# Kernel optimization log

Measured on AMD Instinct MI355X. Metric: run time of the kernel, lower is better.

Reference implementation:

```python
import jax, jax.numpy as jnp
import numpy as np

HEADS = 8
DIM_HEAD = 64
SCALE = DIM_HEAD ** -0.5


def setup_inputs() -> dict:
    key = jax.random.key(0)
    k1, k2, k3, k4 = jax.random.split(key, 4)
    b, dim, l = 4, 256, 2048
    hidden = HEADS * DIM_HEAD  # 512
    x = jax.random.normal(k1, (b, dim, l), dtype=jnp.float32)
    w_qkv = jax.random.normal(k2, (3 * hidden, dim), dtype=jnp.float32) * (dim ** -0.5)
    w_out = jax.random.normal(k3, (dim, hidden), dtype=jnp.float32) * (hidden ** -0.5)
    b_out = jax.random.normal(k4, (dim,), dtype=jnp.float32) * 0.01
    return {"x": x, "w_qkv": w_qkv, "w_out": w_out, "b_out": b_out}


def reference(x, w_qkv, w_out, b_out):
    b, c, l = x.shape
    hidden = HEADS * DIM_HEAD
    # 1x1 conv == pointwise linear over channels
    qkv = jnp.einsum('oc,bcl->bol', w_qkv, x)  # [b, 3*hidden, l]
    q, k, v = jnp.split(qkv, 3, axis=1)
    def to_heads(t):
        return t.reshape(b, HEADS, DIM_HEAD, l)  # b h d l
    q, k, v = to_heads(q), to_heads(k), to_heads(v)
    q = q * SCALE
    sim = jnp.einsum('bhdi,bhdj->bhij', q, k)      # [b, h, l, l]
    attn = jax.nn.softmax(sim, axis=-1)
    out = jnp.einsum('bhij,bhdj->bhid', attn, v)   # [b, h, l, d]
    out = out.transpose(0, 1, 3, 2).reshape(b, hidden, l)  # b (h d) l
    return jnp.einsum('oc,bcl->bol', w_out, out) + b_out[None, :, None]
```

## Files before the change

### kernel.cpp

```cpp
#include <hip/hip_runtime.h>
#include <math.h>

#define Bn   4
#define Cc   256
#define Ll   2048
#define Hh   8
#define Dd   64
#define HID  512
#define OQKV 1536

typedef _Float16 half4v __attribute__((ext_vector_type(4)));
typedef _Float16 half8v __attribute__((ext_vector_type(8)));
typedef float    f32x16 __attribute__((ext_vector_type(16)));

__global__ __launch_bounds__(256) void conv_w(const float* __restrict__ wqkv,
                                              const float* __restrict__ wout,
                                              _Float16* __restrict__ wqkvh,
                                              _Float16* __restrict__ wouth) {
  int idx = blockIdx.x * 256 + threadIdx.x;
  int stride = gridDim.x * 256;
  for (int i = idx; i < OQKV * Cc; i += stride) {
    float v = wqkv[i];
    if (i < HID * Cc) v *= 0.125f;
    wqkvh[i] = (_Float16)v;
  }
  for (int i = idx; i < Cc * HID; i += stride) wouth[i] = (_Float16)wout[i];
}

__global__ __launch_bounds__(256) void conv_xT(const float* __restrict__ x,
                                               _Float16* __restrict__ xT) {
  __shared__ _Float16 T[64][72];
  const int l0 = blockIdx.x * 64, c0 = blockIdx.y * 64, bz = blockIdx.z;
  const int t = threadIdx.x;
  const float* xb = x + ((size_t)bz * Cc + c0) * Ll + l0;
  {
    int cl = t >> 2;
    int lq = (t & 3) * 16;
#pragma unroll
    for (int i = 0; i < 16; i += 4) {
      float4 v = *(const float4*)&xb[(size_t)cl * Ll + lq + i];
      T[lq + i + 0][cl] = (_Float16)v.x;
      T[lq + i + 1][cl] = (_Float16)v.y;
      T[lq + i + 2][cl] = (_Float16)v.z;
      T[lq + i + 3][cl] = (_Float16)v.w;
    }
  }
  __syncthreads();
  {
    int ll = t >> 2;
    int cq = (t & 3) * 16;
    _Float16* dst = xT + ((size_t)bz * Ll + l0 + ll) * Cc + c0 + cq;
    *(half8v*)&dst[0] = *(const half8v*)&T[ll][cq];
    *(half8v*)&dst[8] = *(const half8v*)&T[ll][cq + 8];
  }
}

template <int MODE>
__global__ __launch_bounds__(256) void gemm_f16(
    const _Float16* __restrict__ A, const _Float16* __restrict__ B,
    const float* __restrict__ bias, void* __restrict__ C, int M, int K) {
  __shared__ _Float16 As[128][40];
  __shared__ _Float16 Bs[128][40];
  const int bz = blockIdx.z;
  const int m0 = blockIdx.y * 128, n0 = blockIdx.x * 128;
  const int t = threadIdx.x;
  const int w = t >> 6, lane = t & 63, lid = lane & 31, lh = lane >> 5;
  const int mw = (w >> 1) * 64, nw = (w & 1) * 64;
  const _Float16* Bb = B + (size_t)bz * Ll * K;

  f32x16 acc[2][2];
#pragma unroll
  for (int a = 0; a < 2; ++a)
#pragma unroll
    for (int b2 = 0; b2 < 2; ++b2)
#pragma unroll
      for (int r = 0; r < 16; ++r) acc[a][b2][r] = 0.0f;

  for (int k0 = 0; k0 < K; k0 += 32) {
    for (int c = t; c < 512; c += 256) {
      int row = c >> 2, kc = (c & 3) * 8;
      *(half8v*)&As[row][kc] = *(const half8v*)&A[(size_t)(m0 + row) * K + k0 + kc];
      *(half8v*)&Bs[row][kc] = *(const half8v*)&Bb[(size_t)(n0 + row) * K + k0 + kc];
    }
    __syncthreads();
#pragma unroll
    for (int kq = 0; kq < 2; ++kq) {
      half8v af[2], bf[2];
#pragma unroll
      for (int ms = 0; ms < 2; ++ms)
        af[ms] = *(const half8v*)&As[mw + ms * 32 + lid][kq * 16 + 8 * lh];
#pragma unroll
      for (int ns = 0; ns < 2; ++ns)
        bf[ns] = *(const half8v*)&Bs[nw + ns * 32 + lid][kq * 16 + 8 * lh];
#pragma unroll
      for (int ms = 0; ms < 2; ++ms)
#pragma unroll
        for (int ns = 0; ns < 2; ++ns)
          acc[ms][ns] = __builtin_amdgcn_mfma_f32_32x32x16_f16(af[ms], bf[ns], acc[ms][ns], 0, 0, 0);
    }
    __syncthreads();
  }
#pragma unroll
  for (int ms = 0; ms < 2; ++ms)
#pragma unroll
    for (int ns = 0; ns < 2; ++ns)
#pragma unroll
      for (int r = 0; r < 16; ++r) {
        int row = m0 + mw + ms * 32 + (r & 3) + 8 * (r >> 2) + 4 * lh;
        int col = n0 + nw + ns * 32 + lid;
        float v = acc[ms][ns][r];
        if (MODE == 1) {
          ((float*)C)[((size_t)bz * M + row) * Ll + col] = v + bias[row];
        } else {
          ((_Float16*)C)[((size_t)bz * M + row) * Ll + col] = (_Float16)v;
        }
      }
}

__global__ __launch_bounds__(256) void attn_f16(const _Float16* __restrict__ qkv,
                                                _Float16* __restrict__ aoutT) {
  const int b = blockIdx.z, h = blockIdx.y;
  const int i0 = blockIdx.x * 128;
  const int t = threadIdx.x;
  const int w = t >> 6, lane = t & 63, lid = lane & 31, lh = lane >> 5;
  const _Float16* qb = qkv + ((size_t)b * OQKV + h * Dd) * Ll;
  const _Float16* kb = qb + (size_t)HID * Ll;
  const _Float16* vb = qb + (size_t)(2 * HID) * Ll;

  __shared__ _Float16 Qs[128][72];
  __shared__ _Float16 Ks[64][72];
  __shared__ _Float16 Vs[64][72];
  __shared__ _Float16 Ps[128][72];

  {
    int il4 = (t & 15) * 4;
    int dl = (t >> 4) * 4;
#pragma unroll
    for (int half2 = 0; half2 < 2; ++half2) {
      int il = half2 * 64 + il4;
      half4v rows[4];
#pragma unroll
      for (int r = 0; r < 4; ++r)
        rows[r] = *(const half4v*)&qb[(size_t)(dl + r) * Ll + i0 + il];
#pragma unroll
      for (int c = 0; c < 4; ++c) {
        half4v o;
        o[0] = rows[0][c]; o[1] = rows[1][c]; o[2] = rows[2][c]; o[3] = rows[3][c];
        *(half4v*)&Qs[il + c][dl] = o;
      }
    }
  }
  __syncthreads();

  half8v qf[4];
#pragma unroll
  for (int kq = 0; kq < 4; ++kq)
    qf[kq] = *(const half8v*)&Qs[32 * w + lid][kq * 16 + 8 * lh];

  float lsum = 0.0f;
  f32x16 oacc[2];
#pragma unroll
  for (int ds = 0; ds < 2; ++ds)
#pragma unroll
    for (int r = 0; r < 16; ++r) oacc[ds][r] = 0.0f;

  for (int j0 = 0; j0 < Ll; j0 += 64) {
    __syncthreads();
    {
      int jl = (t & 15) * 4, dl = (t >> 4) * 4;
      half4v rows[4];
#pragma unroll
      for (int r = 0; r < 4; ++r)
        rows[r] = *(const half4v*)&kb[(size_t)(dl + r) * Ll + j0 + jl];
#pragma unroll
      for (int c = 0; c < 4; ++c) {
        half4v o;
        o[0] = rows[0][c]; o[1] = rows[1][c]; o[2] = rows[2][c]; o[3] = rows[3][c];
        *(half4v*)&Ks[jl + c][dl] = o;
      }
    }
    {
      int dl = t >> 2, jl = (t & 3) * 16;
      *(half8v*)&Vs[dl][jl]     = *(const half8v*)&vb[(size_t)dl * Ll + j0 + jl];
      *(half8v*)&Vs[dl][jl + 8] = *(const half8v*)&vb[(size_t)dl * Ll + j0 + jl + 8];
    }
    __syncthreads();

#pragma unroll
    for (int ms = 0; ms < 2; ++ms) {
      f32x16 s;
#pragma unroll
      for (int r = 0; r < 16; ++r) s[r] = 0.0f;
#pragma unroll
      for (int kq = 0; kq < 4; ++kq) {
        half8v kf = *(const half8v*)&Ks[ms * 32 + lid][kq * 16 + 8 * lh];
        s = __builtin_amdgcn_mfma_f32_32x32x16_f16(kf, qf[kq], s, 0, 0, 0);
      }
#pragma unroll
      for (int g = 0; g < 4; ++g) {
        half4v pk;
#pragma unroll
        for (int c = 0; c < 4; ++c) {
          float p = __expf(s[4 * g + c] - 3.0f);
          lsum += p;
          pk[c] = (_Float16)p;
        }
        *(half4v*)&Ps[32 * w + lid][ms * 32 + 8 * g + 4 * lh] = pk;
      }
    }
    __syncthreads();

#pragma unroll
    for (int ds = 0; ds < 2; ++ds)
#pragma unroll
      for (int jq = 0; jq < 4; ++jq) {
        half8v vf = *(const half8v*)&Vs[ds * 32 + lid][jq * 16 + 8 * lh];
        half8v pf = *(const half8v*)&Ps[32 * w + lid][jq * 16 + 8 * lh];
        oacc[ds] = __builtin_amdgcn_mfma_f32_32x32x16_f16(vf, pf, oacc[ds], 0, 0, 0);
      }
  }

  lsum += __shfl_xor(lsum, 32);
  float inv = 1.0f / lsum;
  _Float16* dst = aoutT + ((size_t)b * Ll + i0 + 32 * w + lid) * HID + h * Dd;
#pragma unroll
  for (int ds = 0; ds < 2; ++ds)
#pragma unroll
    for (int g = 0; g < 4; ++g) {
      int d = ds * 32 + 8 * g + 4 * lh;
      half4v o;
#pragma unroll
      for (int c = 0; c < 4; ++c) o[c] = (_Float16)(oacc[ds][4 * g + c] * inv);
      *(half4v*)&dst[d] = o;
    }
}

extern "C" void kernel_launch(void* const* d_in, const int* in_sizes, int n_in,
                              void* d_out, int out_size, void* d_ws, size_t ws_size,
                              hipStream_t stream) {
  const float* x     = (const float*)d_in[0];
  const float* w_qkv = (const float*)d_in[1];
  const float* w_out = (const float*)d_in[2];
  const float* b_out = (const float*)d_in[3];
  float* out = (float*)d_out;

  char* ws = (char*)d_ws;
  _Float16* xT     = (_Float16*)(ws);
  _Float16* wqkvh  = (_Float16*)(ws + 4194304);
  _Float16* wouth  = (_Float16*)(ws + 4980736);
  _Float16* qkvh   = (_Float16*)(ws + 5242880);
  _Float16* aoutT  = (_Float16*)(ws + 30408704);

  dim3 blk(256);
  conv_w<<<512, blk, 0, stream>>>(w_qkv, w_out, wqkvh, wouth);
  conv_xT<<<dim3(Ll / 64, Cc / 64, Bn), blk, 0, stream>>>(x, xT);
  gemm_f16<0><<<dim3(Ll / 128, OQKV / 128, Bn), blk, 0, stream>>>(
      wqkvh, xT, nullptr, qkvh, OQKV, Cc);
  attn_f16<<<dim3(Ll / 128, Hh, Bn), blk, 0, stream>>>(qkvh, aoutT);
  gemm_f16<1><<<dim3(Ll / 128, Cc / 128, Bn), blk, 0, stream>>>(
      wouth, aoutT, b_out, out, Cc, HID);
}
```

Measured before the change: 162.8 us.

## Double-buffer K/V in attention, keep P in registers, swizzle LDS, fuse conversions

The attention kernel now double-buffers the K and V tiles: the next tile's global loads are issued into registers before the current tile's MFMAs and written to LDS afterwards, so there is one barrier per iteration instead of three. The P shared-memory round trip is removed by packing the exp results to fp16 and exchanging halves between lanes with shuffles so they form the B operand directly. Q and K tiles get an XOR swizzle to cut LDS bank conflicts, and s_setprio hints are placed around the MFMA blocks. The weight and x conversion kernels are merged into one launch, at the cost of more registers and LDS per block, which may lower occupancy.

```diff
diff --git a/kernel.cpp b/kernel.cpp
--- a/kernel.cpp
+++ b/kernel.cpp
@@ -13,25 +13,25 @@
 typedef _Float16 half8v __attribute__((ext_vector_type(8)));
 typedef float    f32x16 __attribute__((ext_vector_type(16)));
 
-__global__ __launch_bounds__(256) void conv_w(const float* __restrict__ wqkv,
-                                              const float* __restrict__ wout,
-                                              _Float16* __restrict__ wqkvh,
-                                              _Float16* __restrict__ wouth) {
-  int idx = blockIdx.x * 256 + threadIdx.x;
-  int stride = gridDim.x * 256;
-  for (int i = idx; i < OQKV * Cc; i += stride) {
-    float v = wqkv[i];
-    if (i < HID * Cc) v *= 0.125f;
-    wqkvh[i] = (_Float16)v;
-  }
-  for (int i = idx; i < Cc * HID; i += stride) wouth[i] = (_Float16)wout[i];
-}
-
-__global__ __launch_bounds__(256) void conv_xT(const float* __restrict__ x,
-                                               _Float16* __restrict__ xT) {
+__global__ __launch_bounds__(256) void conv_xTw(const float* __restrict__ x,
+                                                const float* __restrict__ wqkv,
+                                                const float* __restrict__ wout,
+                                                _Float16* __restrict__ xT,
+                                                _Float16* __restrict__ wqkvh,
+                                                _Float16* __restrict__ wouth) {
   __shared__ _Float16 T[64][72];
   const int l0 = blockIdx.x * 64, c0 = blockIdx.y * 64, bz = blockIdx.z;
   const int t = threadIdx.x;
+  {
+    int gid = (((blockIdx.z * gridDim.y + blockIdx.y) * gridDim.x + blockIdx.x) << 8) + t;
+    int nthr = (gridDim.x * gridDim.y * gridDim.z) << 8;
+    for (int i = gid; i < OQKV * Cc; i += nthr) {
+      float v = wqkv[i];
+      if (i < HID * Cc) v *= 0.125f;
+      wqkvh[i] = (_Float16)v;
+    }
+    for (int i = gid; i < Cc * HID; i += nthr) wouth[i] = (_Float16)wout[i];
+  }
   const float* xb = x + ((size_t)bz * Cc + c0) * Ll + l0;
   {
     int cl = t >> 2;
@@ -117,6 +117,12 @@
       }
 }
 
+__device__ inline unsigned pkh(float a, float b) {
+  union { _Float16 h[2]; unsigned u; } x;
+  x.h[0] = (_Float16)a; x.h[1] = (_Float16)b;
+  return x.u;
+}
+
 __global__ __launch_bounds__(256) void attn_f16(const _Float16* __restrict__ qkv,
                                                 _Float16* __restrict__ aoutT) {
   const int b = blockIdx.z, h = blockIdx.y;
@@ -128,13 +134,13 @@
   const _Float16* vb = qb + (size_t)(2 * HID) * Ll;
 
   __shared__ _Float16 Qs[128][72];
-  __shared__ _Float16 Ks[64][72];
-  __shared__ _Float16 Vs[64][72];
-  __shared__ _Float16 Ps[128][72];
+  __shared__ _Float16 Ks[2][64][72];
+  __shared__ _Float16 Vs[2][64][72];
 
   {
     int il4 = (t & 15) * 4;
     int dl = (t >> 4) * 4;
+    int cc = dl >> 3, cs = dl & 7;
 #pragma unroll
     for (int half2 = 0; half2 < 2; ++half2) {
       int il = half2 * 64 + il4;
@@ -146,16 +152,36 @@
       for (int c = 0; c < 4; ++c) {
         half4v o;
         o[0] = rows[0][c]; o[1] = rows[1][c]; o[2] = rows[2][c]; o[3] = rows[3][c];
-        *(half4v*)&Qs[il + c][dl] = o;
-      }
-    }
+        int row = il + c;
+        *(half4v*)&Qs[row][((cc ^ ((row >> 2) & 7)) << 3) | cs] = o;
+      }
+    }
+  }
+  {
+    int jl = (t & 15) * 4, dl = (t >> 4) * 4;
+    int cc = dl >> 3, cs = dl & 7;
+    half4v rows[4];
+#pragma unroll
+    for (int r = 0; r < 4; ++r)
+      rows[r] = *(const half4v*)&kb[(size_t)(dl + r) * Ll + jl];
+#pragma unroll
+    for (int c = 0; c < 4; ++c) {
+      half4v o;
+      o[0] = rows[0][c]; o[1] = rows[1][c]; o[2] = rows[2][c]; o[3] = rows[3][c];
+      int row = jl + c;
+      *(half4v*)&Ks[0][row][((cc ^ ((row >> 2) & 7)) << 3) | cs] = o;
+    }
+    int dv = t >> 2, jv = (t & 3) * 16;
+    *(half8v*)&Vs[0][dv][jv]     = *(const half8v*)&vb[(size_t)dv * Ll + jv];
+    *(half8v*)&Vs[0][dv][jv + 8] = *(const half8v*)&vb[(size_t)dv * Ll + jv + 8];
   }
   __syncthreads();
 
+  const int key = (lid >> 2) & 7;
   half8v qf[4];
 #pragma unroll
   for (int kq = 0; kq < 4; ++kq)
-    qf[kq] = *(const half8v*)&Qs[32 * w + lid][kq * 16 + 8 * lh];
+    qf[kq] = *(const half8v*)&Qs[32 * w + lid][((2 * kq + lh) ^ key) << 3];
 
   float lsum = 0.0f;
   f32x16 oacc[2];
@@ -164,60 +190,84 @@
 #pragma unroll
     for (int r = 0; r < 16; ++r) oacc[ds][r] = 0.0f;
 
+  const int kjl = (t & 15) * 4, kdl = (t >> 4) * 4;
+  const int kcc = kdl >> 3, kcs = kdl & 7;
+  const int vdl = t >> 2, vjl = (t & 3) * 16;
+
   for (int j0 = 0; j0 < Ll; j0 += 64) {
-    __syncthreads();
-    {
-      int jl = (t & 15) * 4, dl = (t >> 4) * 4;
-      half4v rows[4];
+    const int cur = (j0 >> 6) & 1;
+    const int nj = j0 + 64;
+    const bool more = nj < Ll;
+
+    half4v krows[4];
+    half8v vr0, vr1;
+    if (more) {
 #pragma unroll
       for (int r = 0; r < 4; ++r)
-        rows[r] = *(const half4v*)&kb[(size_t)(dl + r) * Ll + j0 + jl];
+        krows[r] = *(const half4v*)&kb[(size_t)(kdl + r) * Ll + nj + kjl];
+      vr0 = *(const half8v*)&vb[(size_t)vdl * Ll + nj + vjl];
+      vr1 = *(const half8v*)&vb[(size_t)vdl * Ll + nj + vjl + 8];
+    }
+
+#pragma unroll
+    for (int ms = 0; ms < 2; ++ms) {
+      f32x16 s;
+#pragma unroll
+      for (int r = 0; r < 16; ++r) s[r] = 0.0f;
+      const int krow = ms * 32 + lid;
+      __builtin_amdgcn_s_setprio(1);
+#pragma unroll
+      for (int kq = 0; kq < 4; ++kq) {
+        half8v kf = *(const half8v*)&Ks[cur][krow][((2 * kq + lh) ^ key) << 3];
+        s = __builtin_amdgcn_mfma_f32_32x32x16_f16(kf, qf[kq], s, 0, 0, 0);
+      }
+      __builtin_amdgcn_s_setprio(0);
+      unsigned W[8];
+#pragma unroll
+      for (int q = 0; q < 4; ++q) {
+        float p0 = __expf(s[4 * q + 0] - 3.0f);
+        float p1 = __expf(s[4 * q + 1] - 3.0f);
+        float p2 = __expf(s[4 * q + 2] - 3.0f);
+        float p3 = __expf(s[4 * q + 3] - 3.0f);
+        lsum += (p0 + p1) + (p2 + p3);
+        W[2 * q]     = pkh(p0, p1);
+        W[2 * q + 1] = pkh(p2, p3);
+      }
+#pragma unroll
+      for (int f = 0; f < 2; ++f) {
+        unsigned s0 = lh ? W[4 * f + 0] : W[4 * f + 2];
+        unsigned s1 = lh ? W[4 * f + 1] : W[4 * f + 3];
+        unsigned r0 = (unsigned)__shfl_xor((int)s0, 32);
+        unsigned r1 = (unsigned)__shfl_xor((int)s1, 32);
+        union { unsigned u[4]; half8v hv; } pu;
+        pu.u[0] = lh ? r0 : W[4 * f + 0];
+        pu.u[1] = lh ? r1 : W[4 * f + 1];
+        pu.u[2] = lh ? W[4 * f + 2] : r0;
+        pu.u[3] = lh ? W[4 * f + 3] : r1;
+        const int jq = 2 * ms + f;
+        __builtin_amdgcn_s_setprio(1);
+#pragma unroll
+        for (int ds = 0; ds < 2; ++ds) {
+          half8v vf = *(const half8v*)&Vs[cur][ds * 32 + lid][jq * 16 + 8 * lh];
+          oacc[ds] = __builtin_amdgcn_mfma_f32_32x32x16_f16(vf, pu.hv, oacc[ds], 0, 0, 0);
+        }
+        __builtin_amdgcn_s_setprio(0);
+      }
+    }
+
+    if (more) {
+      const int nb = cur ^ 1;
 #pragma unroll
       for (int c = 0; c < 4; ++c) {
         half4v o;
-        o[0] = rows[0][c]; o[1] = rows[1][c]; o[2] = rows[2][c]; o[3] = rows[3][c];
-        *(half4v*)&Ks[jl + c][dl] = o;
-      }
-    }
-    {
-      int dl = t >> 2, jl = (t & 3) * 16;
-      *(half8v*)&Vs[dl][jl]     = *(const half8v*)&vb[(size_t)dl * Ll + j0 + jl];
-      *(half8v*)&Vs[dl][jl + 8] = *(const half8v*)&vb[(size_t)dl * Ll + j0 + jl + 8];
-    }
-    __syncthreads();
-
-#pragma unroll
-    for (int ms = 0; ms < 2; ++ms) {
-      f32x16 s;
-#pragma unroll
-      for (int r = 0; r < 16; ++r) s[r] = 0.0f;
-#pragma unroll
-      for (int kq = 0; kq < 4; ++kq) {
-        half8v kf = *(const half8v*)&Ks[ms * 32 + lid][kq * 16 + 8 * lh];
-        s = __builtin_amdgcn_mfma_f32_32x32x16_f16(kf, qf[kq], s, 0, 0, 0);
-      }
-#pragma unroll
-      for (int g = 0; g < 4; ++g) {
-        half4v pk;
-#pragma unroll
-        for (int c = 0; c < 4; ++c) {
-          float p = __expf(s[4 * g + c] - 3.0f);
-          lsum += p;
-          pk[c] = (_Float16)p;
-        }
-        *(half4v*)&Ps[32 * w + lid][ms * 32 + 8 * g + 4 * lh] = pk;
-      }
-    }
-    __syncthreads();
-
-#pragma unroll
-    for (int ds = 0; ds < 2; ++ds)
-#pragma unroll
-      for (int jq = 0; jq < 4; ++jq) {
-        half8v vf = *(const half8v*)&Vs[ds * 32 + lid][jq * 16 + 8 * lh];
-        half8v pf = *(const half8v*)&Ps[32 * w + lid][jq * 16 + 8 * lh];
-        oacc[ds] = __builtin_amdgcn_mfma_f32_32x32x16_f16(vf, pf, oacc[ds], 0, 0, 0);
-      }
+        o[0] = krows[0][c]; o[1] = krows[1][c]; o[2] = krows[2][c]; o[3] = krows[3][c];
+        int row = kjl + c;
+        *(half4v*)&Ks[nb][row][((kcc ^ ((row >> 2) & 7)) << 3) | kcs] = o;
+      }
+      *(half8v*)&Vs[nb][vdl][vjl]     = vr0;
+      *(half8v*)&Vs[nb][vdl][vjl + 8] = vr1;
+      __syncthreads();
+    }
   }
 
   lsum += __shfl_xor(lsum, 32);
@@ -252,8 +302,7 @@
   _Float16* aoutT  = (_Float16*)(ws + 30408704);
 
   dim3 blk(256);
-  conv_w<<<512, blk, 0, stream>>>(w_qkv, w_out, wqkvh, wouth);
-  conv_xT<<<dim3(Ll / 64, Cc / 64, Bn), blk, 0, stream>>>(x, xT);
+  conv_xTw<<<dim3(Ll / 64, Cc / 64, Bn), blk, 0, stream>>>(x, w_qkv, w_out, xT, wqkvh, wouth);
   gemm_f16<0><<<dim3(Ll / 128, OQKV / 128, Bn), blk, 0, stream>>>(
       wqkvh, xT, nullptr, qkvh, OQKV, Cc);
   attn_f16<<<dim3(Ll / 128, Hh, Bn), blk, 0, stream>>>(qkvh, aoutT);
```

Measured after the change: 163.0 us. Within noise of the previous version (+0.1%).
